# Kernel optimization log

Hardware: AMD Instinct MI355X
Metric: run time of the kernel (lower is better)

Reference implementation:

```python
import jax, jax.numpy as jnp
import numpy as np
from jax import lax

D_MODEL = 1024
D_INNER = 2048   # expand * d_model
D_STATE = 16
DT_RANK = 128    # ceil(d_inner / 16)
K = 4            # depthwise conv kernel size
EPS = 1e-5


def setup_inputs() -> dict:
    key = jax.random.key(0)
    ks = jax.random.split(key, 12)
    x = jax.random.normal(ks[0], (2, 1024, D_MODEL), dtype=jnp.float32)
    norm_w = jnp.ones((D_MODEL,), jnp.float32)
    norm_b = jnp.zeros((D_MODEL,), jnp.float32)
    # linear weights stored (in, out)
    in_proj_w = jax.random.normal(ks[1], (D_MODEL, 2 * D_INNER), jnp.float32) * (D_MODEL ** -0.5)
    conv_w = jax.random.normal(ks[2], (D_INNER, K), jnp.float32) * (K ** -0.5)
    conv_b = jnp.zeros((D_INNER,), jnp.float32)
    x_proj_w = jax.random.normal(ks[3], (D_INNER, DT_RANK + 2 * D_STATE), jnp.float32) * (D_INNER ** -0.5)
    dt_init_std = DT_RANK ** -0.5
    dt_proj_w = jax.random.uniform(ks[4], (DT_RANK, D_INNER), jnp.float32, -dt_init_std, dt_init_std)
    dt = jnp.exp(jax.random.uniform(ks[5], (D_INNER,), jnp.float32)
                 * (np.log(0.1) - np.log(0.001)) + np.log(0.001))
    dt_proj_b = dt + jnp.log(-jnp.expm1(-dt))  # inverse-softplus init
    A_log = jax.random.normal(ks[6], (D_INNER, D_STATE), jnp.float32)
    D_param = jax.random.normal(ks[7], (D_INNER,), jnp.float32)
    out_proj_w = jax.random.normal(ks[8], (D_INNER, D_MODEL), jnp.float32) * (D_INNER ** -0.5)
    return dict(x=x, norm_w=norm_w, norm_b=norm_b, in_proj_w=in_proj_w,
                conv_w=conv_w, conv_b=conv_b, x_proj_w=x_proj_w,
                dt_proj_w=dt_proj_w, dt_proj_b=dt_proj_b, A_log=A_log,
                D_param=D_param, out_proj_w=out_proj_w)


def _layer_norm(x, w, b):
    mu = jnp.mean(x, axis=-1, keepdims=True)
    var = jnp.mean(jnp.square(x - mu), axis=-1, keepdims=True)
    return (x - mu) * lax.rsqrt(var + EPS) * w + b


def _causal_depthwise_conv(x, w, b):
    # x: (B, L, D); w: (D, K). Equivalent to torch conv1d(pad=3)[:, :, :L].
    L = x.shape[1]
    xp = jnp.pad(x, ((0, 0), (K - 1, 0), (0, 0)))
    out = b
    for k in range(K):
        out = out + w[:, k] * xp[:, k:k + L, :]
    return out


def _selective_scan(u, delta, A, B, C, D):
    # u, delta: (B, L, D); A: (D, N); B, C: (B, L, N); D: (D,)
    deltaA = jnp.exp(jnp.einsum('bld,dn->bldn', delta, A))           # (B,L,D,N)
    deltaBu = jnp.einsum('bld,bln,bld->bldn', delta, B, u)           # (B,L,D,N)
    bsz, _, d, n = deltaA.shape

    def step(h, inp):
        dA, dBu, Ct = inp
        h = dA * h + dBu                                             # (B,D,N)
        y = jnp.einsum('bdn,bn->bd', h, Ct)
        return h, y

    h0 = jnp.zeros((bsz, d, n), u.dtype)
    _, ys = lax.scan(step, h0,
                     (deltaA.transpose(1, 0, 2, 3),
                      deltaBu.transpose(1, 0, 2, 3),
                      C.transpose(1, 0, 2)))
    y = ys.transpose(1, 0, 2)                                        # (B,L,D)
    return y + u * D


def reference(x, norm_w, norm_b, in_proj_w, conv_w, conv_b, x_proj_w,
              dt_proj_w, dt_proj_b, A_log, D_param, out_proj_w):
    residual = x
    h = _layer_norm(x, norm_w, norm_b)
    xr = h @ in_proj_w                                               # (B,L,2*D_inner)
    xs, res = xr[..., :D_INNER], xr[..., D_INNER:]
    xs = _causal_depthwise_conv(xs, conv_w, conv_b)
    xs = jax.nn.silu(xs)
    # S6
    A = -jnp.exp(A_log)
    xp = xs @ x_proj_w                                               # (B,L,dt_rank+2N)
    dr = xp[..., :DT_RANK]
    Bm = xp[..., DT_RANK:DT_RANK + D_STATE]
    Cm = xp[..., DT_RANK + D_STATE:]
    delta = jax.nn.softplus(dr @ dt_proj_w + dt_proj_b)
    y = _selective_scan(xs, delta, A, Bm, Cm, D_param)
    y = y * jax.nn.silu(res)
    return y @ out_proj_w + residual
```

## Files before the change

kernel.cpp:

```cpp
#include <hip/hip_runtime.h>
#include <hip/hip_bf16.h>
#include <math.h>

#define BSZ     2
#define LLEN    1024
#define DM      1024
#define DI      2048
#define DS      16
#define DTR     128
#define NXP     160
#define MROWS   (BSZ*LLEN)
#define NCH     32
#define CHL     (LLEN/NCH)

typedef short  bf16x8 __attribute__((ext_vector_type(8)));
typedef float  f32x4  __attribute__((ext_vector_type(4)));

__device__ __forceinline__ unsigned short f2bf(float f) {
    unsigned int u = __float_as_uint(f);
    return (unsigned short)((u + 0x7FFFu + ((u >> 16) & 1u)) >> 16);
}

__global__ __launch_bounds__(256) void ln_bf16(
    const float* __restrict__ x, const float* __restrict__ w,
    const float* __restrict__ b, unsigned short* __restrict__ hb)
{
    const int r = blockIdx.x;
    const int tid = threadIdx.x;
    const float4 v = ((const float4*)(x + (size_t)r * DM))[tid];
    float s  = v.x + v.y + v.z + v.w;
    float q  = v.x*v.x + v.y*v.y + v.z*v.z + v.w*v.w;
    #pragma unroll
    for (int o = 32; o > 0; o >>= 1) {
        s += __shfl_down(s, o);
        q += __shfl_down(q, o);
    }
    __shared__ float ss[4], sq[4];
    if ((tid & 63) == 0) { ss[tid >> 6] = s; sq[tid >> 6] = q; }
    __syncthreads();
    s = ss[0] + ss[1] + ss[2] + ss[3];
    q = sq[0] + sq[1] + sq[2] + sq[3];
    const float mu  = s * (1.0f / DM);
    const float var = q * (1.0f / DM) - mu * mu;
    const float rs  = rsqrtf(var + 1e-5f);
    const float4 wv = ((const float4*)w)[tid];
    const float4 bv = ((const float4*)b)[tid];
    ushort4 ob;
    ob.x = f2bf((v.x - mu) * rs * wv.x + bv.x);
    ob.y = f2bf((v.y - mu) * rs * wv.y + bv.y);
    ob.z = f2bf((v.z - mu) * rs * wv.z + bv.z);
    ob.w = f2bf((v.w - mu) * rs * wv.w + bv.w);
    *(ushort4*)&hb[(size_t)r * DM + (tid << 2)] = ob;
}

__global__ __launch_bounds__(256) void cast_transpose_g(
    const float* __restrict__ src, unsigned short* __restrict__ dst,
    int K, int N)
{
    __shared__ unsigned short t[64][68];
    const int tid = threadIdx.x;
    const int k0 = blockIdx.y * 64, n0 = blockIdx.x * 64;
    #pragma unroll
    for (int q = 0; q < 4; ++q) {
        int idx = q * 256 + tid;
        int r = idx >> 4, c = (idx & 15) * 4;
        if (k0 + r < K) {
            #pragma unroll
            for (int e = 0; e < 4; ++e)
                if (n0 + c + e < N)
                    t[r][c + e] = f2bf(src[(size_t)(k0 + r) * N + n0 + c + e]);
        }
    }
    __syncthreads();
    #pragma unroll
    for (int q = 0; q < 4; ++q) {
        int idx = q * 256 + tid;
        int r = idx >> 4, c = (idx & 15) * 4;
        if (n0 + r < N) {
            #pragma unroll
            for (int e = 0; e < 4; ++e)
                if (k0 + c + e < K)
                    dst[(size_t)(n0 + r) * K + k0 + c + e] = t[c + e][r];
        }
    }
}

template<int BM, int BN, int EPI>
__global__ __launch_bounds__(256) void gemm_bf16(
    const unsigned short* __restrict__ A,
    const unsigned short* __restrict__ Bt,
    float* __restrict__ C, int M, int N, int K, int kpb,
    const float* __restrict__ bias,
    const float* __restrict__ resid)
{
    constexpr int LDT = 72;
    __shared__ unsigned short As[BM][LDT];
    __shared__ unsigned short Bs[BN][LDT];
    const int tid  = threadIdx.x;
    const int m0   = blockIdx.y * BM;
    const int n0   = blockIdx.x * BN;
    const int kbeg = blockIdx.z * kpb;
    const int kend = kbeg + kpb;
    float* Cw = C + (size_t)blockIdx.z * M * N;
    const int wave = tid >> 6;
    const int lane = tid & 63;
    const int wr   = (wave >> 1) * (BM / 2);
    const int wc   = (wave & 1) * (BN / 2);
    constexpr int FM = BM / 32;
    constexpr int FN = BN / 32;
    const int l15 = lane & 15;
    const int kg  = lane >> 4;

    f32x4 acc[FM][FN] = {};

    for (int kt = kbeg; kt < kend; kt += 64) {
        __syncthreads();
        #pragma unroll
        for (int q = 0; q < BM / 32; ++q) {
            int idx = q * 256 + tid;
            int r = idx >> 3, c = (idx & 7) * 8;
            *(uint4*)&As[r][c] = *(const uint4*)&A[(size_t)(m0 + r) * K + kt + c];
        }
        #pragma unroll
        for (int q = 0; q < BN / 32; ++q) {
            int idx = q * 256 + tid;
            int r = idx >> 3, c = (idx & 7) * 8;
            *(uint4*)&Bs[r][c] = *(const uint4*)&Bt[(size_t)(n0 + r) * K + kt + c];
        }
        __syncthreads();
        #pragma unroll
        for (int ks = 0; ks < 2; ++ks) {
            bf16x8 af[FM], bfr[FN];
            #pragma unroll
            for (int i = 0; i < FM; ++i)
                af[i] = *(const bf16x8*)&As[wr + i * 16 + l15][ks * 32 + kg * 8];
            #pragma unroll
            for (int j = 0; j < FN; ++j)
                bfr[j] = *(const bf16x8*)&Bs[wc + j * 16 + l15][ks * 32 + kg * 8];
            #pragma unroll
            for (int i = 0; i < FM; ++i)
                #pragma unroll
                for (int j = 0; j < FN; ++j)
                    acc[i][j] = __builtin_amdgcn_mfma_f32_16x16x32_bf16(
                        af[i], bfr[j], acc[i][j], 0, 0, 0);
        }
    }
    #pragma unroll
    for (int i = 0; i < FM; ++i) {
        #pragma unroll
        for (int j = 0; j < FN; ++j) {
            const int row = m0 + wr + i * 16 + kg * 4;
            const int col = n0 + wc + j * 16 + l15;
            #pragma unroll
            for (int r = 0; r < 4; ++r) {
                float v = acc[i][j][r];
                if (EPI == 1) {
                    float t = v + bias[col];
                    v = (t > 20.f) ? t : log1pf(__expf(t));
                } else if (EPI == 2) {
                    v += resid[(size_t)(row + r) * N + col];
                }
                Cw[(size_t)(row + r) * N + col] = v;
            }
        }
    }
}

__global__ __launch_bounds__(256) void xproj_reduce(
    const float* __restrict__ P4, float* __restrict__ xp,
    unsigned short* __restrict__ drb)
{
    const int idx = blockIdx.x * 256 + threadIdx.x;
    float s = 0.f;
    #pragma unroll
    for (int j = 0; j < 4; ++j)
        s += P4[(size_t)j * (MROWS * NXP) + idx];
    xp[idx] = s;
    const int row = idx / NXP, col = idx - row * NXP;
    if (col < DTR) drb[(size_t)row * DTR + col] = f2bf(s);
}

__global__ __launch_bounds__(256) void conv_silu(
    const float* __restrict__ xr, const float* __restrict__ cw,
    const float* __restrict__ cb, float* __restrict__ xs,
    unsigned short* __restrict__ xsb, float* __restrict__ g)
{
    const int idx = blockIdx.x * 256 + threadIdx.x;
    const int d = idx & (DI - 1);
    const int t = (idx >> 11) & (LLEN - 1);
    const int b = idx >> 21;
    const float4 wv = ((const float4*)cw)[d];
    const float w[4] = {wv.x, wv.y, wv.z, wv.w};
    float acc = cb[d];
    #pragma unroll
    for (int k = 0; k < 4; ++k) {
        const int tt = t + k - 3;
        if (tt >= 0)
            acc = fmaf(w[k], xr[((size_t)(b * LLEN + tt) << 12) + d], acc);
    }
    const float sig = 1.f / (1.f + __expf(-acc));
    const float v = acc * sig;
    xs[idx] = v;
    xsb[idx] = f2bf(v);
    const float r = xr[((size_t)(b * LLEN + t) << 12) + DI + d];
    g[idx] = r / (1.f + __expf(-r));
}

__global__ __launch_bounds__(256) void scan_ps(
    const float* __restrict__ delta, const float* __restrict__ xs,
    const float* __restrict__ xp, const float* __restrict__ A_log,
    float* __restrict__ S, float* __restrict__ sdlt)
{
    const int blk  = blockIdx.x;
    const int dgrp = blk & 7;
    const int j    = (blk >> 3) & (NCH - 1);
    const int b    = blk >> 8;
    const int d    = dgrp * 256 + threadIdx.x;
    float aL[DS], h[DS];
    #pragma unroll
    for (int n = 0; n < DS; ++n) {
        aL[n] = -__expf(A_log[d * DS + n]) * 1.44269504088896f;
        h[n] = 0.f;
    }
    float sd = 0.f;
    const int t0 = j * CHL;
    for (int t = t0; t < t0 + CHL; ++t) {
        const size_t row = (size_t)(b * LLEN + t);
        const float dlt = delta[row * DI + d];
        const float du  = dlt * xs[row * DI + d];
        sd += dlt;
        const float* Bp = &xp[row * NXP + DTR];
        #pragma unroll
        for (int n = 0; n < DS; ++n) {
            const float dA = exp2f(dlt * aL[n]);
            h[n] = fmaf(dA, h[n], du * Bp[n]);
        }
    }
    float* So = &S[(((size_t)j * BSZ + b) * DI + d) * DS];
    #pragma unroll
    for (int n = 0; n < DS; ++n) So[n] = h[n];
    sdlt[((size_t)j * BSZ + b) * DI + d] = sd;
}

__global__ __launch_bounds__(256) void scan_fix(
    float* __restrict__ S, const float* __restrict__ sdlt,
    const float* __restrict__ A_log)
{
    const int c = blockIdx.x * 256 + threadIdx.x;
    const int n = c & 15;
    const int d = (c >> 4) & (DI - 1);
    const int b = c >> 15;
    const float aL = -__expf(A_log[d * DS + n]) * 1.44269504088896f;
    float h = 0.f;
    #pragma unroll
    for (int j = 0; j < NCH; ++j) {
        const size_t base = ((size_t)j * BSZ + b) * DI + d;
        const float Pj = exp2f(aL * sdlt[base]);
        const float Sj = S[base * DS + n];
        S[base * DS + n] = h;
        h = fmaf(Pj, h, Sj);
    }
}

__global__ __launch_bounds__(256) void scan_y(
    const float* __restrict__ delta, const float* __restrict__ xs,
    const float* __restrict__ xp, const float* __restrict__ g,
    const float* __restrict__ A_log, const float* __restrict__ Dp,
    const float* __restrict__ H0, unsigned short* __restrict__ yb)
{
    const int blk  = blockIdx.x;
    const int dgrp = blk & 7;
    const int j    = (blk >> 3) & (NCH - 1);
    const int b    = blk >> 8;
    const int d    = dgrp * 256 + threadIdx.x;
    float aL[DS], h[DS];
    const float* H = &H0[(((size_t)j * BSZ + b) * DI + d) * DS];
    #pragma unroll
    for (int n = 0; n < DS; ++n) {
        aL[n] = -__expf(A_log[d * DS + n]) * 1.44269504088896f;
        h[n] = H[n];
    }
    const float Dd = Dp[d];
    const int t0 = j * CHL;
    for (int t = t0; t < t0 + CHL; ++t) {
        const size_t row = (size_t)(b * LLEN + t);
        const float dlt = delta[row * DI + d];
        const float u   = xs[row * DI + d];
        const float du  = dlt * u;
        const float* Bp = &xp[row * NXP + DTR];
        const float* Cp = Bp + DS;
        float y = Dd * u;
        #pragma unroll
        for (int n = 0; n < DS; ++n) {
            const float dA = exp2f(dlt * aL[n]);
            h[n] = fmaf(dA, h[n], du * Bp[n]);
            y = fmaf(h[n], Cp[n], y);
        }
        yb[row * DI + d] = f2bf(y * g[row * DI + d]);
    }
}

extern "C" void kernel_launch(void* const* d_in, const int* in_sizes, int n_in,
                              void* d_out, int out_size, void* d_ws, size_t ws_size,
                              hipStream_t stream)
{
    (void)in_sizes; (void)n_in; (void)out_size; (void)ws_size;
    const float* x         = (const float*)d_in[0];
    const float* norm_w    = (const float*)d_in[1];
    const float* norm_b    = (const float*)d_in[2];
    const float* in_proj_w = (const float*)d_in[3];
    const float* conv_w    = (const float*)d_in[4];
    const float* conv_b    = (const float*)d_in[5];
    const float* x_proj_w  = (const float*)d_in[6];
    const float* dt_proj_w = (const float*)d_in[7];
    const float* dt_proj_b = (const float*)d_in[8];
    const float* A_log     = (const float*)d_in[9];
    const float* D_param   = (const float*)d_in[10];
    const float* out_proj_w= (const float*)d_in[11];
    float* out = (float*)d_out;

    char* ws = (char*)d_ws;
    float*          xr    = (float*)(ws);
    float*          P4    = (float*)(ws);
    float*          delta = (float*)(ws);
    float*          Sbuf  = (float*)(ws + 16777216);
    float*          xp    = (float*)(ws + 25165824);
    unsigned short* drb   = (unsigned short*)(ws + 27262976);
    float*          sdlt  = (float*)(ws + 27787264);
    float*          xs    = (float*)(ws + 33554432);
    float*          g     = (float*)(ws + 50331648);
    unsigned short* wInT  = (unsigned short*)(ws + 50331648);
    unsigned short* hb    = (unsigned short*)(ws + 58720256);
    unsigned short* wOutT = (unsigned short*)(ws + 58720256);
    unsigned short* xsb   = (unsigned short*)(ws + 67108864);
    unsigned short* yb    = (unsigned short*)(ws + 67108864);
    unsigned short* wXT   = (unsigned short*)(ws + 75497472);
    unsigned short* dtwT  = (unsigned short*)(ws + 76152832);

    ln_bf16<<<MROWS, 256, 0, stream>>>(x, norm_w, norm_b, hb);

    cast_transpose_g<<<dim3(64, 16), 256, 0, stream>>>(in_proj_w, wInT, DM, 2 * DI);
    cast_transpose_g<<<dim3(3, 32), 256, 0, stream>>>(x_proj_w, wXT, DI, NXP);
    cast_transpose_g<<<dim3(32, 2), 256, 0, stream>>>(dt_proj_w, dtwT, DTR, DI);

    gemm_bf16<128, 128, 0><<<dim3(32, 16, 1), 256, 0, stream>>>(
        hb, wInT, xr, MROWS, 2 * DI, DM, DM, nullptr, nullptr);

    conv_silu<<<(BSZ * LLEN * DI) / 256, 256, 0, stream>>>(
        xr, conv_w, conv_b, xs, xsb, g);

    gemm_bf16<128, 32, 0><<<dim3(5, 16, 4), 256, 0, stream>>>(
        xsb, wXT, P4, MROWS, NXP, DI, DI / 4, nullptr, nullptr);
    xproj_reduce<<<(MROWS * NXP) / 256, 256, 0, stream>>>(P4, xp, drb);

    gemm_bf16<128, 128, 1><<<dim3(16, 16, 1), 256, 0, stream>>>(
        drb, dtwT, delta, MROWS, DI, DTR, DTR, dt_proj_b, nullptr);

    scan_ps<<<BSZ * NCH * (DI / 256), 256, 0, stream>>>(
        delta, xs, xp, A_log, Sbuf, sdlt);
    scan_fix<<<(BSZ * DI * DS) / 256, 256, 0, stream>>>(Sbuf, sdlt, A_log);
    scan_y<<<BSZ * NCH * (DI / 256), 256, 0, stream>>>(
        delta, xs, xp, g, A_log, D_param, Sbuf, yb);

    cast_transpose_g<<<dim3(16, 32), 256, 0, stream>>>(out_proj_w, wOutT, DI, DM);

    gemm_bf16<128, 64, 2><<<dim3(16, 16, 1), 256, 0, stream>>>(
        yb, wOutT, out, MROWS, DM, DI, DI, nullptr, x);
}
```

Baseline: 220.7 us.

## Restructure chunked scan into local-y plus state correction; add direct-to-LDS GEMM

The chunked selective scan now computes the intra-chunk output y (with zero initial state) in the first pass and stores it in place over delta. The running cumulative delta is stored in place over xs. The final pass no longer re-runs the 16-state recurrence; it adds a correction term C·(H0·exp(A·cumdelta)) to the partial y. The in_proj GEMM is also replaced by a new kernel that uses global_load_lds to move tiles straight into LDS with a fixed 128x128x64 tiling. The trade-off is an extra output write per element in the first pass and the in-place buffer reuse, in exchange for cutting the recurrence work in the second pass.

```diff
diff --git a/kernel.cpp b/kernel.cpp
--- a/kernel.cpp
+++ b/kernel.cpp
@@ -19,6 +19,12 @@
 __device__ __forceinline__ unsigned short f2bf(float f) {
     unsigned int u = __float_as_uint(f);
     return (unsigned short)((u + 0x7FFFu + ((u >> 16) & 1u)) >> 16);
+}
+
+__device__ __forceinline__ void gload_lds16(const void* g, void* lds) {
+    __builtin_amdgcn_global_load_lds(
+        (const __attribute__((address_space(1))) void*)g,
+        (__attribute__((address_space(3))) void*)lds, 16, 0, 0);
 }
 
 __global__ __launch_bounds__(256) void ln_bf16(
@@ -81,6 +87,68 @@
             for (int e = 0; e < 4; ++e)
                 if (k0 + c + e < K)
                     dst[(size_t)(n0 + r) * K + k0 + c + e] = t[c + e][r];
+        }
+    }
+}
+
+__global__ __launch_bounds__(256) void gemm_gl(
+    const unsigned short* __restrict__ A,
+    const unsigned short* __restrict__ Bt,
+    float* __restrict__ C, int M, int N, int K)
+{
+    __shared__ unsigned short As[128][64];
+    __shared__ unsigned short Bs[128][64];
+    const int tid  = threadIdx.x;
+    const int m0   = blockIdx.y * 128;
+    const int n0   = blockIdx.x * 128;
+    const int wave = tid >> 6;
+    const int lane = tid & 63;
+    const int wr   = (wave >> 1) * 64;
+    const int wc   = (wave & 1) * 64;
+    const int l15  = lane & 15;
+    const int kg   = lane >> 4;
+    const int lrow = lane >> 3;
+    const int lcol = (lane & 7) * 8;
+
+    f32x4 acc[4][4] = {};
+
+    for (int kt = 0; kt < K; kt += 64) {
+        __syncthreads();
+        #pragma unroll
+        for (int q = 0; q < 4; ++q) {
+            const int rbase = wave * 32 + q * 8;
+            gload_lds16(&A[(size_t)(m0 + rbase + lrow) * K + kt + lcol],
+                        &As[rbase][0]);
+            gload_lds16(&Bt[(size_t)(n0 + rbase + lrow) * K + kt + lcol],
+                        &Bs[rbase][0]);
+        }
+        __syncthreads();
+        #pragma unroll
+        for (int ks = 0; ks < 2; ++ks) {
+            bf16x8 af[4], bfr[4];
+            #pragma unroll
+            for (int i = 0; i < 4; ++i)
+                af[i] = *(const bf16x8*)&As[wr + i * 16 + l15][ks * 32 + kg * 8];
+            #pragma unroll
+            for (int j = 0; j < 4; ++j)
+                bfr[j] = *(const bf16x8*)&Bs[wc + j * 16 + l15][ks * 32 + kg * 8];
+            #pragma unroll
+            for (int i = 0; i < 4; ++i)
+                #pragma unroll
+                for (int j = 0; j < 4; ++j)
+                    acc[i][j] = __builtin_amdgcn_mfma_f32_16x16x32_bf16(
+                        af[i], bfr[j], acc[i][j], 0, 0, 0);
+        }
+    }
+    #pragma unroll
+    for (int i = 0; i < 4; ++i) {
+        #pragma unroll
+        for (int j = 0; j < 4; ++j) {
+            const int row = m0 + wr + i * 16 + kg * 4;
+            const int col = n0 + wc + j * 16 + l15;
+            #pragma unroll
+            for (int r = 0; r < 4; ++r)
+                C[(size_t)(row + r) * N + col] = acc[i][j][r];
         }
     }
 }
@@ -206,10 +274,10 @@
     g[idx] = r / (1.f + __expf(-r));
 }
 
-__global__ __launch_bounds__(256) void scan_ps(
-    const float* __restrict__ delta, const float* __restrict__ xs,
+__global__ __launch_bounds__(256) void scan_part(
+    float* __restrict__ dio, float* __restrict__ xio,
     const float* __restrict__ xp, const float* __restrict__ A_log,
-    float* __restrict__ S, float* __restrict__ sdlt)
+    const float* __restrict__ Dp, float* __restrict__ S)
 {
     const int blk  = blockIdx.x;
     const int dgrp = blk & 7;
@@ -222,28 +290,34 @@
         aL[n] = -__expf(A_log[d * DS + n]) * 1.44269504088896f;
         h[n] = 0.f;
     }
+    const float Dd = Dp[d];
     float sd = 0.f;
     const int t0 = j * CHL;
     for (int t = t0; t < t0 + CHL; ++t) {
         const size_t row = (size_t)(b * LLEN + t);
-        const float dlt = delta[row * DI + d];
-        const float du  = dlt * xs[row * DI + d];
+        const float dlt = dio[row * DI + d];
+        const float u   = xio[row * DI + d];
+        const float du  = dlt * u;
         sd += dlt;
         const float* Bp = &xp[row * NXP + DTR];
+        const float* Cp = Bp + DS;
+        float y = Dd * u;
         #pragma unroll
         for (int n = 0; n < DS; ++n) {
             const float dA = exp2f(dlt * aL[n]);
             h[n] = fmaf(dA, h[n], du * Bp[n]);
-        }
+            y = fmaf(h[n], Cp[n], y);
+        }
+        dio[row * DI + d] = y;
+        xio[row * DI + d] = sd;
     }
     float* So = &S[(((size_t)j * BSZ + b) * DI + d) * DS];
     #pragma unroll
     for (int n = 0; n < DS; ++n) So[n] = h[n];
-    sdlt[((size_t)j * BSZ + b) * DI + d] = sd;
 }
 
 __global__ __launch_bounds__(256) void scan_fix(
-    float* __restrict__ S, const float* __restrict__ sdlt,
+    float* __restrict__ S, const float* __restrict__ cumD,
     const float* __restrict__ A_log)
 {
     const int c = blockIdx.x * 256 + threadIdx.x;
@@ -254,48 +328,43 @@
     float h = 0.f;
     #pragma unroll
     for (int j = 0; j < NCH; ++j) {
-        const size_t base = ((size_t)j * BSZ + b) * DI + d;
-        const float Pj = exp2f(aL * sdlt[base]);
-        const float Sj = S[base * DS + n];
-        S[base * DS + n] = h;
+        const float sd = cumD[(size_t)(b * LLEN + j * CHL + CHL - 1) * DI + d];
+        const size_t base = (((size_t)j * BSZ + b) * DI + d) * DS + n;
+        const float Pj = exp2f(aL * sd);
+        const float Sj = S[base];
+        S[base] = h;
         h = fmaf(Pj, h, Sj);
     }
 }
 
-__global__ __launch_bounds__(256) void scan_y(
-    const float* __restrict__ delta, const float* __restrict__ xs,
+__global__ __launch_bounds__(256) void scan_corr(
+    const float* __restrict__ yp, const float* __restrict__ cumD,
     const float* __restrict__ xp, const float* __restrict__ g,
-    const float* __restrict__ A_log, const float* __restrict__ Dp,
-    const float* __restrict__ H0, unsigned short* __restrict__ yb)
+    const float* __restrict__ A_log, const float* __restrict__ H0,
+    unsigned short* __restrict__ yb)
 {
     const int blk  = blockIdx.x;
     const int dgrp = blk & 7;
     const int j    = (blk >> 3) & (NCH - 1);
     const int b    = blk >> 8;
     const int d    = dgrp * 256 + threadIdx.x;
-    float aL[DS], h[DS];
-    const float* H = &H0[(((size_t)j * BSZ + b) * DI + d) * DS];
+    float aL[DS], H[DS];
+    const float* Hp = &H0[(((size_t)j * BSZ + b) * DI + d) * DS];
     #pragma unroll
     for (int n = 0; n < DS; ++n) {
         aL[n] = -__expf(A_log[d * DS + n]) * 1.44269504088896f;
-        h[n] = H[n];
-    }
-    const float Dd = Dp[d];
+        H[n] = Hp[n];
+    }
     const int t0 = j * CHL;
     for (int t = t0; t < t0 + CHL; ++t) {
         const size_t row = (size_t)(b * LLEN + t);
-        const float dlt = delta[row * DI + d];
-        const float u   = xs[row * DI + d];
-        const float du  = dlt * u;
-        const float* Bp = &xp[row * NXP + DTR];
-        const float* Cp = Bp + DS;
-        float y = Dd * u;
-        #pragma unroll
-        for (int n = 0; n < DS; ++n) {
-            const float dA = exp2f(dlt * aL[n]);
-            h[n] = fmaf(dA, h[n], du * Bp[n]);
-            y = fmaf(h[n], Cp[n], y);
-        }
+        const float cd = cumD[row * DI + d];
+        const float* Cp = &xp[row * NXP + DTR + DS];
+        float corr = 0.f;
+        #pragma unroll
+        for (int n = 0; n < DS; ++n)
+            corr = fmaf(H[n] * exp2f(aL[n] * cd), Cp[n], corr);
+        const float y = yp[row * DI + d] + corr;
         yb[row * DI + d] = f2bf(y * g[row * DI + d]);
     }
 }
@@ -326,7 +395,6 @@
     float*          Sbuf  = (float*)(ws + 16777216);
     float*          xp    = (float*)(ws + 25165824);
     unsigned short* drb   = (unsigned short*)(ws + 27262976);
-    float*          sdlt  = (float*)(ws + 27787264);
     float*          xs    = (float*)(ws + 33554432);
     float*          g     = (float*)(ws + 50331648);
     unsigned short* wInT  = (unsigned short*)(ws + 50331648);
@@ -343,8 +411,7 @@
     cast_transpose_g<<<dim3(3, 32), 256, 0, stream>>>(x_proj_w, wXT, DI, NXP);
     cast_transpose_g<<<dim3(32, 2), 256, 0, stream>>>(dt_proj_w, dtwT, DTR, DI);
 
-    gemm_bf16<128, 128, 0><<<dim3(32, 16, 1), 256, 0, stream>>>(
-        hb, wInT, xr, MROWS, 2 * DI, DM, DM, nullptr, nullptr);
+    gemm_gl<<<dim3(32, 16), 256, 0, stream>>>(hb, wInT, xr, MROWS, 2 * DI, DM);
 
     conv_silu<<<(BSZ * LLEN * DI) / 256, 256, 0, stream>>>(
         xr, conv_w, conv_b, xs, xsb, g);
@@ -356,11 +423,11 @@
     gemm_bf16<128, 128, 1><<<dim3(16, 16, 1), 256, 0, stream>>>(
         drb, dtwT, delta, MROWS, DI, DTR, DTR, dt_proj_b, nullptr);
 
-    scan_ps<<<BSZ * NCH * (DI / 256), 256, 0, stream>>>(
-        delta, xs, xp, A_log, Sbuf, sdlt);
-    scan_fix<<<(BSZ * DI * DS) / 256, 256, 0, stream>>>(Sbuf, sdlt, A_log);
-    scan_y<<<BSZ * NCH * (DI / 256), 256, 0, stream>>>(
-        delta, xs, xp, g, A_log, D_param, Sbuf, yb);
+    scan_part<<<BSZ * NCH * (DI / 256), 256, 0, stream>>>(
+        delta, xs, xp, A_log, D_param, Sbuf);
+    scan_fix<<<(BSZ * DI * DS) / 256, 256, 0, stream>>>(Sbuf, xs, A_log);
+    scan_corr<<<BSZ * NCH * (DI / 256), 256, 0, stream>>>(
+        delta, xs, xp, g, A_log, Sbuf, yb);
 
     cast_transpose_g<<<dim3(16, 32), 256, 0, stream>>>(out_proj_w, wOutT, DI, DM);
 
```

After: 227.9 us. 1.03x slower.
